# Kernel optimization log

Measured on AMD Instinct MI355X. Metric: run time of the kernel, lower is better.

## Reference

```python
import jax, jax.numpy as jnp
import numpy as np
import math

DIM_V = 512
NUM_HEADS = 8
LN_EPS = 1e-5


def _layer_norm(x, g, b):
    mu = jnp.mean(x, axis=-1, keepdims=True)
    var = jnp.mean(jnp.square(x - mu), axis=-1, keepdims=True)
    return (x - mu) * jax.lax.rsqrt(var + LN_EPS) * g + b


def setup_inputs() -> dict:
    key = jax.random.key(0)
    ks = jax.random.split(key, 12)
    B, Nq, Nk, Dq, Dk, Dv = 16, 1024, 1024, 512, 512, DIM_V
    s_q = 1.0 / math.sqrt(Dq)
    s_k = 1.0 / math.sqrt(Dk)
    s_v = 1.0 / math.sqrt(Dv)
    return {
        "Q": jax.random.normal(ks[0], (B, Nq, Dq), jnp.float32),
        "K": jax.random.normal(ks[1], (B, Nk, Dk), jnp.float32),
        "Wq": jax.random.normal(ks[2], (Dq, Dv), jnp.float32) * s_q,
        "bq": jnp.zeros((Dv,), jnp.float32),
        "Wk": jax.random.normal(ks[3], (Dk, Dv), jnp.float32) * s_k,
        "bk": jnp.zeros((Dv,), jnp.float32),
        "Wv": jax.random.normal(ks[4], (Dk, Dv), jnp.float32) * s_k,
        "bv": jnp.zeros((Dv,), jnp.float32),
        "Wo": jax.random.normal(ks[5], (Dv, Dv), jnp.float32) * s_v,
        "bo": jnp.zeros((Dv,), jnp.float32),
        "g0": jnp.ones((Dv,), jnp.float32),
        "b0": jnp.zeros((Dv,), jnp.float32),
        "g1": jnp.ones((Dv,), jnp.float32),
        "b1": jnp.zeros((Dv,), jnp.float32),
    }


def reference(Q, K, Wq, bq, Wk, bk, Wv, bv, Wo, bo, g0, b0, g1, b1):
    B, Nq, _ = Q.shape
    H = NUM_HEADS
    hd = DIM_V // H
    Qp = Q @ Wq + bq            # [B, Nq, Dv]
    Kp = K @ Wk + bk            # [B, Nk, Dv]
    Vp = K @ Wv + bv            # [B, Nk, Dv]
    # split heads: [B, N, H, hd]
    Qh = Qp.reshape(B, Nq, H, hd)
    Kh = Kp.reshape(B, -1, H, hd)
    Vh = Vp.reshape(B, -1, H, hd)
    # NOTE: original scales by sqrt(dim_V), not sqrt(head_dim)
    scores = jnp.einsum("bqhd,bkhd->bhqk", Qh, Kh) / math.sqrt(DIM_V)
    A = jax.nn.softmax(scores, axis=-1)          # [B, H, Nq, Nk]
    Oh = Qh + jnp.einsum("bhqk,bkhd->bqhd", A, Vh)  # residual on projected Q
    O = Oh.reshape(B, Nq, DIM_V)
    O = _layer_norm(O, g0, b0)
    O = O + jax.nn.relu(O @ Wo + bo)
    O = _layer_norm(O, g1, b1)
    return O
```

## Files before the change

### kernel.cpp

```cpp
#include <hip/hip_runtime.h>
#include <hip/hip_bf16.h>

typedef float f32x4 __attribute__((ext_vector_type(4)));
typedef float f32x16 __attribute__((ext_vector_type(16)));
typedef __bf16 bf16x8 __attribute__((ext_vector_type(8)));
typedef __bf16 bf16x4 __attribute__((ext_vector_type(4)));

#define MFMA(a, b, c) __builtin_amdgcn_mfma_f32_16x16x32_bf16(a, b, c, 0, 0, 0)
#define MFMA32(a, b, c) __builtin_amdgcn_mfma_f32_32x32x16_bf16(a, b, c, 0, 0, 0)
#define AS1 __attribute__((address_space(1)))
#define AS3 __attribute__((address_space(3)))

__device__ __forceinline__ void gload16(const void* g, void* l) {
    __builtin_amdgcn_global_load_lds((const AS1 unsigned int*)g, (AS3 unsigned int*)l, 16, 0, 0);
}

__device__ __forceinline__ unsigned short f2bf(float f) {
    union { float f; unsigned u; } x{f};
    unsigned r = x.u + 0x7FFFu + ((x.u >> 16) & 1u);
    return (unsigned short)(r >> 16);
}
__device__ __forceinline__ float bf2f(unsigned short u) {
    union { unsigned u; float f; } x; x.u = ((unsigned)u) << 16; return x.f;
}
__device__ __forceinline__ unsigned pkbf(float a, float b) {
    union { __bf16 h[2]; unsigned u; } r;
    r.h[0] = (__bf16)a; r.h[1] = (__bf16)b;
    return r.u;
}

__global__ __launch_bounds__(256) void k_pack4(const float* W0, const float* W1,
                                               const float* W2, const float* W3,
                                               unsigned short* P0, unsigned short* P1,
                                               unsigned short* P2, unsigned short* P3) {
    __shared__ float T[64][65];
    int sel = blockIdx.x >> 6, tile = blockIdx.x & 63;
    const float* W = sel == 0 ? W0 : sel == 1 ? W1 : sel == 2 ? W2 : W3;
    unsigned short* Wp = sel == 0 ? P0 : sel == 1 ? P1 : sel == 2 ? P2 : P3;
    int k0 = (tile >> 3) * 64, n0 = (tile & 7) * 64;
    int tid = threadIdx.x;
    for (int it = 0; it < 16; ++it) {
        int id = it * 256 + tid;
        int r = id >> 6, c = id & 63;
        T[r][c] = W[(k0 + r) * 512 + n0 + c];
    }
    __syncthreads();
    if (sel < 3) {
        #pragma unroll
        for (int cc = 0; cc < 2; ++cc) {
            int ch = cc * 256 + tid;
            int ksl = ch >> 8, n16l = (ch >> 6) & 3, ln = ch & 63;
            int kg = ln >> 4, nl = ln & 15;
            union { unsigned short u[8]; int4 v; } tmp;
            #pragma unroll
            for (int e = 0; e < 8; ++e)
                tmp.u[e] = f2bf(T[ksl * 32 + kg * 8 + e][n16l * 16 + nl]);
            size_t dst = ((size_t)((k0 >> 5) + ksl) * 32 + (n0 >> 4) + n16l) * 512 + ln * 8;
            *(int4*)(Wp + dst) = tmp.v;
        }
    } else {
        for (int it = 0; it < 16; ++it) {
            int id = it * 256 + tid;
            int r = id >> 6, c = id & 63;
            Wp[(n0 + r) * 512 + k0 + c] = f2bf(T[c][r]);
        }
    }
}

__global__ __launch_bounds__(512, 4) void k_proj3(const float* __restrict__ Qf,
                                                  const float* __restrict__ Kf,
                                                  const unsigned short* __restrict__ WpQ,
                                                  const unsigned short* __restrict__ WpK,
                                                  const unsigned short* __restrict__ WpV,
                                                  const float* __restrict__ bq,
                                                  const float* __restrict__ bk,
                                                  const float* __restrict__ bv,
                                                  unsigned short* __restrict__ Qsc,
                                                  unsigned short* __restrict__ Kp,
                                                  unsigned short* __restrict__ VpT,
                                                  float scale2) {
    __shared__ __align__(16) unsigned short Asm[2][2048];
    const int tid = threadIdx.x, lane = tid & 63, w = tid >> 6;
    const int l15 = lane & 15, l4 = lane >> 4;
    const int bid = blockIdx.x;
    const int sel = bid >> 8, rt = bid & 255;
    const float* A = sel == 0 ? Qf : Kf;
    const unsigned short* Wp = sel == 0 ? WpQ : sel == 1 ? WpK : WpV;
    const int m0 = rt * 64;
    const int wn = w * 64;

    const f32x4 vz = {0.f, 0.f, 0.f, 0.f};
    f32x4 acc[4][4];
    for (int i = 0; i < 4; ++i)
        for (int j = 0; j < 4; ++j) acc[i][j] = vz;

    const int sr = tid >> 3, sc4 = tid & 7;
    const float* aptr = A + (size_t)(m0 + sr) * 512 + sc4 * 4;
    unsigned short* const wdst =
        &Asm[0][0] + sr * 32 + ((sc4 >> 1) ^ (sr & 3)) * 8 + (sc4 & 1) * 4;

    auto WRITEA = [&](const float4& v, int p) {
        union { unsigned u[2]; } r;
        r.u[0] = pkbf(v.x, v.y);
        r.u[1] = pkbf(v.z, v.w);
        *(uint2*)(wdst + p * 2048) = *(uint2*)&r;
    };

    {
        float4 a0 = *(const float4*)(aptr);
        WRITEA(a0, 0);
    }
    __syncthreads();

    const unsigned short* wbase = Wp + (size_t)(w * 4) * 512 + lane * 8;
    if (sel < 2) {
        for (int ks = 0; ks < 16; ++ks) {
            int p = ks & 1;
            float4 anx;
            if (ks < 15) anx = *(const float4*)(aptr + (ks + 1) * 32);
            bf16x8 bfr[4], afr[4];
            #pragma unroll
            for (int j = 0; j < 4; ++j)
                bfr[j] = *(const bf16x8*)(wbase + (size_t)ks * 16384 + j * 512);
            #pragma unroll
            for (int i = 0; i < 4; ++i) {
                int rr = i * 16 + l15;
                afr[i] = *(const bf16x8*)&Asm[p][rr * 32 + (l4 ^ (rr & 3)) * 8];
            }
            __builtin_amdgcn_s_setprio(1);
            #pragma unroll
            for (int i = 0; i < 4; ++i)
                #pragma unroll
                for (int j = 0; j < 4; ++j)
                    acc[i][j] = MFMA(afr[i], bfr[j], acc[i][j]);
            __builtin_amdgcn_s_setprio(0);
            if (ks < 15) WRITEA(anx, p ^ 1);
            __syncthreads();
        }
        const float* bias = sel ? bk : bq;
        unsigned short* out = sel ? Kp : Qsc;
        const float scale = sel ? 1.0f : scale2;
        float bn[4];
        #pragma unroll
        for (int j = 0; j < 4; ++j) bn[j] = bias[wn + j * 16 + l15];
        for (int i = 0; i < 4; ++i)
            for (int j = 0; j < 4; ++j)
                for (int rg = 0; rg < 4; ++rg) {
                    int m = m0 + i * 16 + l4 * 4 + rg;
                    int n = wn + j * 16 + l15;
                    out[(size_t)m * 512 + n] = f2bf((acc[i][j][rg] + bn[j]) * scale);
                }
    } else {
        for (int ks = 0; ks < 16; ++ks) {
            int p = ks & 1;
            float4 anx;
            if (ks < 15) anx = *(const float4*)(aptr + (ks + 1) * 32);
            bf16x8 bfr[4], afr[4];
            #pragma unroll
            for (int j = 0; j < 4; ++j)
                bfr[j] = *(const bf16x8*)(wbase + (size_t)ks * 16384 + j * 512);
            #pragma unroll
            for (int i = 0; i < 4; ++i) {
                int rr = i * 16 + l15;
                afr[i] = *(const bf16x8*)&Asm[p][rr * 32 + (l4 ^ (rr & 3)) * 8];
            }
            __builtin_amdgcn_s_setprio(1);
            #pragma unroll
            for (int i = 0; i < 4; ++i)
                #pragma unroll
                for (int j = 0; j < 4; ++j)
                    acc[i][j] = MFMA(bfr[j], afr[i], acc[i][j]);
            __builtin_amdgcn_s_setprio(0);
            if (ks < 15) WRITEA(anx, p ^ 1);
            __syncthreads();
        }
        const int b = m0 >> 10, key0 = m0 & 1023;
        for (int j = 0; j < 4; ++j) {
            float4 bv4 = *(const float4*)(bv + wn + j * 16 + l4 * 4);
            for (int i = 0; i < 4; ++i)
                for (int rg = 0; rg < 4; ++rg) {
                    int d = wn + j * 16 + l4 * 4 + rg;
                    int key = key0 + i * 16 + l15;
                    VpT[((size_t)(b * 512 + d)) * 1024 + key] = f2bf(acc[i][j][rg] + bv4[rg]);
                }
        }
    }
}

__global__ __launch_bounds__(256, 4) void k_attn32(const unsigned short* __restrict__ Qs,
                                                   const unsigned short* __restrict__ Kp,
                                                   const unsigned short* __restrict__ VpT,
                                                   unsigned short* __restrict__ O1b) {
    __shared__ __align__(16) unsigned short sm[16384];
    const int tid = threadIdx.x, lane = tid & 63, w = tid >> 6;
    const int l31 = lane & 31, hi = lane >> 5;
    int i = blockIdx.x;
    const int xcd = i & 7, jj = i >> 3;
    const int qt = jj & 7, bhl = jj >> 3;
    const int bh = xcd * 16 + bhl;
    const int h = bh & 7, b = bh >> 3;
    const int qrow = b * 1024 + qt * 128 + w * 32 + l31;

    const unsigned short* Ksrc = Kp + (size_t)(b * 1024) * 512 + h * 64;
    const unsigned short* Vsrc = VpT + (size_t)(b * 512 + h * 64) * 1024;
    const unsigned short* qptr = Qs + (size_t)qrow * 512 + h * 64;

    bf16x8 qf[4];
    #pragma unroll
    for (int ks = 0; ks < 4; ++ks)
        qf[ks] = *(const bf16x8*)(qptr + ks * 16 + hi * 8);

    f32x16 acc0, acc1;
    #pragma unroll
    for (int r = 0; r < 16; ++r) { acc0[r] = 0.f; acc1[r] = 0.f; }
    float ls = 0.f;

    auto STAGE = [&](int kv, int p) {
        #pragma unroll
        for (int it = 0; it < 2; ++it) {
            int id = it * 256 + tid;
            int r = id >> 3, x = id & 7, c = x ^ (r & 7);
            unsigned short* ldsb = sm + p * 4096 + (it * 256 + w * 64) * 8;
            gload16(Ksrc + (size_t)(kv * 64 + r) * 512 + c * 8, ldsb);
            gload16(Vsrc + (size_t)r * 1024 + kv * 64 + c * 8, ldsb + 8192);
        }
    };

    STAGE(0, 0);
    __syncthreads();
    for (int kv = 0; kv < 16; ++kv) {
        int p = kv & 1;
        if (kv < 15) STAGE(kv + 1, p ^ 1);
        const unsigned short* Kl = sm + p * 4096;
        const unsigned short* Vl = sm + 8192 + p * 4096;
        const int rsw = (l31 & 7);

        f32x16 s0, s1;
        #pragma unroll
        for (int r = 0; r < 16; ++r) { s0[r] = 0.f; s1[r] = 0.f; }
        __builtin_amdgcn_s_setprio(1);
        #pragma unroll
        for (int ks = 0; ks < 4; ++ks) {
            int c = (2 * ks + hi) ^ rsw;
            bf16x8 kf0 = *(const bf16x8*)&Kl[l31 * 64 + c * 8];
            s0 = MFMA32(kf0, qf[ks], s0);
            bf16x8 kf1 = *(const bf16x8*)&Kl[(32 + l31) * 64 + c * 8];
            s1 = MFMA32(kf1, qf[ks], s1);
        }
        __builtin_amdgcn_s_setprio(0);

        unsigned We[8], Wf[8];
        #pragma unroll
        for (int g = 0; g < 4; ++g) {
            float e0 = __builtin_amdgcn_exp2f(s0[4 * g + 0]);
            float e1 = __builtin_amdgcn_exp2f(s0[4 * g + 1]);
            float e2 = __builtin_amdgcn_exp2f(s0[4 * g + 2]);
            float e3 = __builtin_amdgcn_exp2f(s0[4 * g + 3]);
            float f0 = __builtin_amdgcn_exp2f(s1[4 * g + 0]);
            float f1 = __builtin_amdgcn_exp2f(s1[4 * g + 1]);
            float f2 = __builtin_amdgcn_exp2f(s1[4 * g + 2]);
            float f3 = __builtin_amdgcn_exp2f(s1[4 * g + 3]);
            ls += ((e0 + e1) + (e2 + e3)) + ((f0 + f1) + (f2 + f3));
            We[2 * g + 0] = pkbf(e0, e1); We[2 * g + 1] = pkbf(e2, e3);
            Wf[2 * g + 0] = pkbf(f0, f1); Wf[2 * g + 1] = pkbf(f2, f3);
        }
        bf16x8 pf[4];
        #pragma unroll
        for (int src = 0; src < 2; ++src) {
            const unsigned* W = src == 0 ? We : Wf;
            #pragma unroll
            for (int k2 = 0; k2 < 2; ++k2) {
                unsigned A0 = W[4 * k2 + 0], A1 = W[4 * k2 + 1];
                unsigned B0 = W[4 * k2 + 2], B1 = W[4 * k2 + 3];
                unsigned cross0 = __shfl_xor(hi ? A0 : B0, 32);
                unsigned cross1 = __shfl_xor(hi ? A1 : B1, 32);
                union { unsigned w[4]; bf16x8 v; } r;
                r.w[0] = hi ? cross0 : A0;
                r.w[1] = hi ? cross1 : A1;
                r.w[2] = hi ? B0 : cross0;
                r.w[3] = hi ? B1 : cross1;
                pf[src * 2 + k2] = r.v;
            }
        }

        __builtin_amdgcn_s_setprio(1);
        #pragma unroll
        for (int ks = 0; ks < 4; ++ks) {
            int c = (2 * ks + hi) ^ rsw;
            bf16x8 vf0 = *(const bf16x8*)&Vl[l31 * 64 + c * 8];
            acc0 = MFMA32(vf0, pf[ks], acc0);
            bf16x8 vf1 = *(const bf16x8*)&Vl[(32 + l31) * 64 + c * 8];
            acc1 = MFMA32(vf1, pf[ks], acc1);
        }
        __builtin_amdgcn_s_setprio(0);
        __syncthreads();
    }

    ls += __shfl_xor(ls, 32);
    float linv = 1.0f / ls;
    const float invscale = 15.6841306f;
    unsigned short* orow = O1b + (size_t)qrow * 512 + h * 64;
    #pragma unroll
    for (int g = 0; g < 4; ++g) {
        {
            int d0 = 8 * g + 4 * hi;
            bf16x4 qres = *(const bf16x4*)(qptr + d0);
            bf16x4 ov;
            ov[0] = (__bf16)((float)qres[0] * invscale + acc0[4 * g + 0] * linv);
            ov[1] = (__bf16)((float)qres[1] * invscale + acc0[4 * g + 1] * linv);
            ov[2] = (__bf16)((float)qres[2] * invscale + acc0[4 * g + 2] * linv);
            ov[3] = (__bf16)((float)qres[3] * invscale + acc0[4 * g + 3] * linv);
            *(bf16x4*)(orow + d0) = ov;
        }
        {
            int d0 = 32 + 8 * g + 4 * hi;
            bf16x4 qres = *(const bf16x4*)(qptr + d0);
            bf16x4 ov;
            ov[0] = (__bf16)((float)qres[0] * invscale + acc1[4 * g + 0] * linv);
            ov[1] = (__bf16)((float)qres[1] * invscale + acc1[4 * g + 1] * linv);
            ov[2] = (__bf16)((float)qres[2] * invscale + acc1[4 * g + 2] * linv);
            ov[3] = (__bf16)((float)qres[3] * invscale + acc1[4 * g + 3] * linv);
            *(bf16x4*)(orow + d0) = ov;
        }
    }
}

__global__ __launch_bounds__(256) void k_ln_bf(const unsigned short* __restrict__ in,
                                               unsigned short* __restrict__ outb,
                                               const float* __restrict__ g,
                                               const float* __restrict__ bt) {
    int row = blockIdx.x * 4 + (threadIdx.x >> 6);
    int lane = threadIdx.x & 63;
    const unsigned short* x = in + (size_t)row * 512 + lane * 8;
    bf16x8 v = *(const bf16x8*)x;
    float f[8];
    for (int j = 0; j < 8; ++j) f[j] = (float)v[j];
    float s1 = 0.f, s2 = 0.f;
    for (int j = 0; j < 8; ++j) { s1 += f[j]; s2 += f[j] * f[j]; }
    for (int off = 32; off; off >>= 1) {
        s1 += __shfl_xor(s1, off);
        s2 += __shfl_xor(s2, off);
    }
    float mu = s1 * (1.f / 512.f);
    float var = s2 * (1.f / 512.f) - mu * mu;
    float rs = rsqrtf(var + 1e-5f);
    float4 ga = *(const float4*)(g + lane * 8), gb = *(const float4*)(g + lane * 8 + 4);
    float4 ba = *(const float4*)(bt + lane * 8), bb = *(const float4*)(bt + lane * 8 + 4);
    float gg[8] = {ga.x, ga.y, ga.z, ga.w, gb.x, gb.y, gb.z, gb.w};
    float bv[8] = {ba.x, ba.y, ba.z, ba.w, bb.x, bb.y, bb.z, bb.w};
    bf16x8 y;
    for (int j = 0; j < 8; ++j) y[j] = (__bf16)((f[j] - mu) * rs * gg[j] + bv[j]);
    *(bf16x8*)(outb + (size_t)row * 512 + lane * 8) = y;
}

__global__ __launch_bounds__(512, 2) void k_gemm2ln(const unsigned short* __restrict__ A,
                                                    const unsigned short* __restrict__ Bt,
                                                    const float* __restrict__ bias,
                                                    const float* __restrict__ g1,
                                                    const float* __restrict__ b1,
                                                    float* __restrict__ out) {
    __shared__ __align__(16) unsigned short Ab[2][2048];
    __shared__ __align__(16) unsigned short Bb[2][16384];
    __shared__ float part[64][4][2];
    __shared__ float stats[64][2];
    const int tid = threadIdx.x, lane = tid & 63, w = tid >> 6;
    const int l15 = lane & 15, l4 = lane >> 4;
    const int m0 = blockIdx.x * 64;
    const int wm = (w >> 2) * 32, wn = (w & 3) * 128;

    const f32x4 vz = {0.f, 0.f, 0.f, 0.f};
    f32x4 acc[2][8];
    for (int i = 0; i < 2; ++i)
        for (int j = 0; j < 8; ++j) acc[i][j] = vz;

    const unsigned short* Abase = A + (size_t)m0 * 512;

    auto STAGE = [&](int ks, int p) {
        int kk = ks * 32;
        for (int it = 0; it < 4; ++it) {
            int id = it * 512 + tid;
            int r = id >> 2, x = id & 3, c = x ^ (r & 3);
            gload16(Bt + r * 512 + kk + c * 8, &Bb[p][(it * 512 + w * 64) * 8]);
        }
        if (w < 4) {
            int id = w * 64 + lane;
            int r = id >> 2, x = id & 3, c = x ^ (r & 3);
            gload16(Abase + r * 512 + kk + c * 8, &Ab[p][(w * 64) * 8]);
        }
    };

    STAGE(0, 0);
    __syncthreads();
    for (int ks = 0; ks < 16; ++ks) {
        int p = ks & 1;
        if (ks < 15) STAGE(ks + 1, p ^ 1);
        bf16x8 af[2], bfr[8];
        for (int i = 0; i < 2; ++i) {
            int r = wm + i * 16 + l15, pc = l4 ^ (r & 3);
            af[i] = *(const bf16x8*)&Ab[p][r * 32 + pc * 8];
        }
        for (int j = 0; j < 8; ++j) {
            int r = wn + j * 16 + l15, pc = l4 ^ (r & 3);
            bfr[j] = *(const bf16x8*)&Bb[p][r * 32 + pc * 8];
        }
        __builtin_amdgcn_s_setprio(1);
        for (int i = 0; i < 2; ++i)
            for (int j = 0; j < 8; ++j)
                acc[i][j] = MFMA(af[i], bfr[j], acc[i][j]);
        __builtin_amdgcn_s_setprio(0);
        __syncthreads();
    }

    float bn[8], gv[8], bv2[8];
    for (int j = 0; j < 8; ++j) {
        int n = wn + j * 16 + l15;
        bn[j] = bias[n]; gv[j] = g1[n]; bv2[j] = b1[n];
    }
    f32x4 s1v[2], s2v[2];
    for (int i = 0; i < 2; ++i) { s1v[i] = vz; s2v[i] = vz; }
    for (int i = 0; i < 2; ++i)
        for (int j = 0; j < 8; ++j)
            for (int rg = 0; rg < 4; ++rg) {
                int row = m0 + wm + i * 16 + l4 * 4 + rg;
                int n = wn + j * 16 + l15;
                float z = acc[i][j][rg] + bn[j];
                z = z > 0.f ? z : 0.f;
                float v = bf2f(A[(size_t)row * 512 + n]) + z;
                acc[i][j][rg] = v;
                s1v[i][rg] += v;
                s2v[i][rg] += v * v;
            }
    for (int i = 0; i < 2; ++i)
        for (int rg = 0; rg < 4; ++rg) {
            float a = s1v[i][rg], c = s2v[i][rg];
            for (int off = 1; off < 16; off <<= 1) {
                a += __shfl_xor(a, off);
                c += __shfl_xor(c, off);
            }
            s1v[i][rg] = a; s2v[i][rg] = c;
        }
    if (l15 == 0)
        for (int i = 0; i < 2; ++i)
            for (int rg = 0; rg < 4; ++rg) {
                int rl = wm + i * 16 + l4 * 4 + rg;
                part[rl][w & 3][0] = s1v[i][rg];
                part[rl][w & 3][1] = s2v[i][rg];
            }
    __syncthreads();
    if (tid < 64) {
        float a = 0.f, c = 0.f;
        for (int q = 0; q < 4; ++q) { a += part[tid][q][0]; c += part[tid][q][1]; }
        float mu = a * (1.f / 512.f);
        float var = c * (1.f / 512.f) - mu * mu;
        stats[tid][0] = mu;
        stats[tid][1] = rsqrtf(var + 1e-5f);
    }
    __syncthreads();
    for (int i = 0; i < 2; ++i)
        for (int rg = 0; rg < 4; ++rg) {
            int rl = wm + i * 16 + l4 * 4 + rg;
            float mu = stats[rl][0], rs = stats[rl][1];
            for (int j = 0; j < 8; ++j) {
                int n = wn + j * 16 + l15;
                out[(size_t)(m0 + rl) * 512 + n] = (acc[i][j][rg] - mu) * rs * gv[j] + bv2[j];
            }
        }
}

extern "C" void kernel_launch(void* const* d_in, const int* in_sizes, int n_in,
                              void* d_out, int out_size, void* d_ws, size_t ws_size,
                              hipStream_t stream) {
    const float* Q  = (const float*)d_in[0];
    const float* K  = (const float*)d_in[1];
    const float* Wq = (const float*)d_in[2];
    const float* bq = (const float*)d_in[3];
    const float* Wk = (const float*)d_in[4];
    const float* bk = (const float*)d_in[5];
    const float* Wv = (const float*)d_in[6];
    const float* bv = (const float*)d_in[7];
    const float* Wo = (const float*)d_in[8];
    const float* bo = (const float*)d_in[9];
    const float* g0 = (const float*)d_in[10];
    const float* b0 = (const float*)d_in[11];
    const float* g1 = (const float*)d_in[12];
    const float* b1 = (const float*)d_in[13];
    float* out = (float*)d_out;

    const size_t SZ_BF = (size_t)16384 * 512 * 2;
    const size_t SZ_W  = (size_t)512 * 512 * 2;
    char* p = (char*)d_ws;
    unsigned short* WpQ = (unsigned short*)p; p += SZ_W;
    unsigned short* WpK = (unsigned short*)p; p += SZ_W;
    unsigned short* WpV = (unsigned short*)p; p += SZ_W;
    unsigned short* Wot = (unsigned short*)p; p += SZ_W;
    unsigned short* Qsc = (unsigned short*)p; p += SZ_BF;
    unsigned short* Kp  = (unsigned short*)p; p += SZ_BF;
    unsigned short* VpT = (unsigned short*)p; p += SZ_BF;
    unsigned short* A1b = (unsigned short*)p; p += SZ_BF;
    unsigned short* X0b = (unsigned short*)p; p += SZ_BF;

    k_pack4<<<256, 256, 0, stream>>>(Wq, Wk, Wv, Wo, WpQ, WpK, WpV, Wot);

    const float scale2 = 0.063758718f;
    k_proj3<<<768, 512, 0, stream>>>(Q, K, WpQ, WpK, WpV, bq, bk, bv, Qsc, Kp, VpT, scale2);

    k_attn32<<<1024, 256, 0, stream>>>(Qsc, Kp, VpT, A1b);

    k_ln_bf<<<4096, 256, 0, stream>>>(A1b, X0b, g0, b0);
    k_gemm2ln<<<256, 512, 0, stream>>>(X0b, Wot, bo, g1, b1, out);
}
```

Before: 143.3 us.

## Load projection A operands directly from global, dropping LDS staging and barriers

```diff
diff --git a/kernel.cpp b/kernel.cpp
--- a/kernel.cpp
+++ b/kernel.cpp
@@ -67,7 +67,7 @@
     }
 }
 
-__global__ __launch_bounds__(512, 4) void k_proj3(const float* __restrict__ Qf,
+__global__ __launch_bounds__(512, 2) void k_proj3(const float* __restrict__ Qf,
                                                   const float* __restrict__ Kf,
                                                   const unsigned short* __restrict__ WpQ,
                                                   const unsigned short* __restrict__ WpK,
@@ -79,7 +79,6 @@
                                                   unsigned short* __restrict__ Kp,
                                                   unsigned short* __restrict__ VpT,
                                                   float scale2) {
-    __shared__ __align__(16) unsigned short Asm[2][2048];
     const int tid = threadIdx.x, lane = tid & 63, w = tid >> 6;
     const int l15 = lane & 15, l4 = lane >> 4;
     const int bid = blockIdx.x;
@@ -94,38 +93,22 @@
     for (int i = 0; i < 4; ++i)
         for (int j = 0; j < 4; ++j) acc[i][j] = vz;
 
-    const int sr = tid >> 3, sc4 = tid & 7;
-    const float* aptr = A + (size_t)(m0 + sr) * 512 + sc4 * 4;
-    unsigned short* const wdst =
-        &Asm[0][0] + sr * 32 + ((sc4 >> 1) ^ (sr & 3)) * 8 + (sc4 & 1) * 4;
-
-    auto WRITEA = [&](const float4& v, int p) {
-        union { unsigned u[2]; } r;
-        r.u[0] = pkbf(v.x, v.y);
-        r.u[1] = pkbf(v.z, v.w);
-        *(uint2*)(wdst + p * 2048) = *(uint2*)&r;
-    };
-
-    {
-        float4 a0 = *(const float4*)(aptr);
-        WRITEA(a0, 0);
-    }
-    __syncthreads();
-
+    const float* aptr = A + ((size_t)m0 + l15) * 512 + l4 * 8;
     const unsigned short* wbase = Wp + (size_t)(w * 4) * 512 + lane * 8;
+
     if (sel < 2) {
         for (int ks = 0; ks < 16; ++ks) {
-            int p = ks & 1;
-            float4 anx;
-            if (ks < 15) anx = *(const float4*)(aptr + (ks + 1) * 32);
             bf16x8 bfr[4], afr[4];
             #pragma unroll
             for (int j = 0; j < 4; ++j)
                 bfr[j] = *(const bf16x8*)(wbase + (size_t)ks * 16384 + j * 512);
             #pragma unroll
             for (int i = 0; i < 4; ++i) {
-                int rr = i * 16 + l15;
-                afr[i] = *(const bf16x8*)&Asm[p][rr * 32 + (l4 ^ (rr & 3)) * 8];
+                const float* ap = aptr + (size_t)i * 16 * 512 + ks * 32;
+                f32x4 a0 = *(const f32x4*)ap;
+                f32x4 a1 = *(const f32x4*)(ap + 4);
+                afr[i] = bf16x8{(__bf16)a0[0], (__bf16)a0[1], (__bf16)a0[2], (__bf16)a0[3],
+                                (__bf16)a1[0], (__bf16)a1[1], (__bf16)a1[2], (__bf16)a1[3]};
             }
             __builtin_amdgcn_s_setprio(1);
             #pragma unroll
@@ -134,8 +117,6 @@
                 for (int j = 0; j < 4; ++j)
                     acc[i][j] = MFMA(afr[i], bfr[j], acc[i][j]);
             __builtin_amdgcn_s_setprio(0);
-            if (ks < 15) WRITEA(anx, p ^ 1);
-            __syncthreads();
         }
         const float* bias = sel ? bk : bq;
         unsigned short* out = sel ? Kp : Qsc;
@@ -152,17 +133,17 @@
                 }
     } else {
         for (int ks = 0; ks < 16; ++ks) {
-            int p = ks & 1;
-            float4 anx;
-            if (ks < 15) anx = *(const float4*)(aptr + (ks + 1) * 32);
             bf16x8 bfr[4], afr[4];
             #pragma unroll
             for (int j = 0; j < 4; ++j)
                 bfr[j] = *(const bf16x8*)(wbase + (size_t)ks * 16384 + j * 512);
             #pragma unroll
             for (int i = 0; i < 4; ++i) {
-                int rr = i * 16 + l15;
-                afr[i] = *(const bf16x8*)&Asm[p][rr * 32 + (l4 ^ (rr & 3)) * 8];
+                const float* ap = aptr + (size_t)i * 16 * 512 + ks * 32;
+                f32x4 a0 = *(const f32x4*)ap;
+                f32x4 a1 = *(const f32x4*)(ap + 4);
+                afr[i] = bf16x8{(__bf16)a0[0], (__bf16)a0[1], (__bf16)a0[2], (__bf16)a0[3],
+                                (__bf16)a1[0], (__bf16)a1[1], (__bf16)a1[2], (__bf16)a1[3]};
             }
             __builtin_amdgcn_s_setprio(1);
             #pragma unroll
@@ -171,8 +152,6 @@
                 for (int j = 0; j < 4; ++j)
                     acc[i][j] = MFMA(bfr[j], afr[i], acc[i][j]);
             __builtin_amdgcn_s_setprio(0);
-            if (ks < 15) WRITEA(anx, p ^ 1);
-            __syncthreads();
         }
         const int b = m0 >> 10, key0 = m0 & 1023;
         for (int j = 0; j < 4; ++j) {
```

Result: slower. 194.3 us (+35.6%).
